# Kernel optimization log

Measured on AMD Instinct MI355X. Metric: run time of the kernel, lower is better.

The kernel has to match this reference:

```python
import jax, jax.numpy as jnp
import numpy as np


def setup_inputs() -> dict:
    key = jax.random.key(0)
    k1, k2, k3, k4 = jax.random.split(key, 4)
    num_tokens, hidden = 16384, 7168
    head_dim, coff = 512, 1            # compress_ratio=128 -> coff=1
    compress_ratio = 128
    num_blocks, block_size = 4096, 8   # block_size=8 for compress_ratio=128
    x = jax.random.normal(k1, (num_tokens, hidden), jnp.float32) * 0.02
    W = jax.random.normal(k2, (2 * coff * head_dim, hidden), jnp.float32) * 0.02
    ape = jax.random.normal(k3, (compress_ratio, coff * head_dim), jnp.float32)
    state_cache = jnp.zeros((num_blocks, block_size, 2 * coff * head_dim), jnp.float32)
    positions = jax.random.randint(k4, (num_tokens,), 0, 131072, dtype=jnp.int32)
    slot_mapping = jnp.arange(num_tokens, dtype=jnp.int32)  # unique, in-range slots
    return {"x": x, "W": W, "ape": ape, "state_cache": state_cache,
            "positions": positions, "slot_mapping": slot_mapping, "block_size": 8}


def reference(x, W, ape, state_cache, positions, slot_mapping, block_size):
    # fused_wkv_wgate GEMM (cublas bf16->fp32 in original): [T,H] @ [H,2D] -> [T,2D]
    kv_score = jnp.einsum('th,dh->td', x, W)
    D = W.shape[0] // 2                      # coff * head_dim (state_width)
    kv, score = kv_score[:, :D], kv_score[:, D:]
    compress_ratio = ape.shape[0]
    # fused APE lookup: ape[position % COMPRESS_RATIO] added to score half
    ape_rows = ape[positions % compress_ratio]          # [T, D]
    new_vals = jnp.concatenate([kv, score + ape_rows], axis=-1)  # [T, 2D]
    num_blocks, bs, width = state_cache.shape
    # slot -> (block_idx, pos_in_block) is exactly flat indexing for a
    # contiguous [num_blocks, block_size, width] cache.
    flat = state_cache.reshape(num_blocks * bs, width)
    # slot < 0 tokens are skipped (mapped out of range + mode='drop')
    idx = jnp.where(slot_mapping >= 0, slot_mapping, num_blocks * bs)
    flat = flat.at[idx].set(new_vals, mode='drop')
    return flat.reshape(num_blocks, bs, width)
```

## Files before the change

kernel.cpp:

```cpp
#include <hip/hip_runtime.h>
#include <hip/hip_bf16.h>
#include <stdint.h>


typedef short  bf16x8 __attribute__((ext_vector_type(8)));
typedef float  f32x4  __attribute__((ext_vector_type(4)));

#define BM 128
#define BN 128
#define BK 32
#define NT 256

#define GBM 256
#define GBN 256
#define GBK 64
#define GNT 512

__device__ __forceinline__ uint32_t pack_bf16x2(float lo, float hi) {
    uint32_t a = __float_as_uint(lo);
    uint32_t b = __float_as_uint(hi);
    a += 0x7fffu + ((a >> 16) & 1u);
    b += 0x7fffu + ((b >> 16) & 1u);
    return (a >> 16) | (b & 0xffff0000u);
}

__device__ __forceinline__ void gload_lds16(const uint16_t* g, uint16_t* l) {
    __builtin_amdgcn_global_load_lds(
        (const __attribute__((address_space(1))) uint32_t*)g,
        (__attribute__((address_space(3))) uint32_t*)l,
        16, 0, 0);
}

__global__ void set_flags(const int* __restrict__ slots, uint8_t* __restrict__ flags,
                          int num_tokens, int num_slots) {
    const int i = blockIdx.x * blockDim.x + threadIdx.x;
    if (i < num_tokens) {
        const int s = slots[i];
        if (s >= 0 && s < num_slots) flags[s] = 1;
    }
}

__global__ void prep(const float4* __restrict__ cache, float4* __restrict__ out,
                     const uint8_t* __restrict__ flags,
                     const float4* __restrict__ x, uint4* __restrict__ xb,
                     const float4* __restrict__ w, uint4* __restrict__ wb,
                     int n_c4, int nx8, int nw8) {
    const int i = blockIdx.x * blockDim.x + threadIdx.x;
    if (i < n_c4) {
        if (!flags[i >> 8]) out[i] = cache[i];
    } else if (i < n_c4 + nx8) {
        const int j = i - n_c4;
        const float4 a = x[2 * j];
        const float4 b = x[2 * j + 1];
        uint4 o;
        o.x = pack_bf16x2(a.x, a.y);
        o.y = pack_bf16x2(a.z, a.w);
        o.z = pack_bf16x2(b.x, b.y);
        o.w = pack_bf16x2(b.z, b.w);
        xb[j] = o;
    } else if (i < n_c4 + nx8 + nw8) {
        const int j = i - n_c4 - nx8;
        const float4 a = w[2 * j];
        const float4 b = w[2 * j + 1];
        uint4 o;
        o.x = pack_bf16x2(a.x, a.y);
        o.y = pack_bf16x2(a.z, a.w);
        o.z = pack_bf16x2(b.x, b.y);
        o.w = pack_bf16x2(b.z, b.w);
        wb[j] = o;
    }
}

__global__ __launch_bounds__(GNT, 2)
void gemm_bf16_scatter_256(const uint16_t* __restrict__ XB, const uint16_t* __restrict__ WB,
                           const float* __restrict__ ape, const int* __restrict__ positions,
                           const int* __restrict__ slots, float* __restrict__ out,
                           int K, int D, int CR, int num_slots, int n_tiles_m, int n_tiles_n)
{
    __shared__ uint16_t lds[2 * 2 * GBM * GBK];

    const int t    = threadIdx.x;
    const int lane = t & 63;
    const int wid  = t >> 6;
    const int wr   = wid >> 2;
    const int wc   = wid & 3;
    const int fr   = lane & 15;
    const int fc4  = lane >> 4;

    const int nblk = n_tiles_m * n_tiles_n;
    int tidx = blockIdx.x;
    if ((nblk & 7) == 0) {
        const int per = nblk >> 3;
        tidx = (tidx & 7) * per + (tidx >> 3);
    }
    const int tile_m = tidx / n_tiles_n;
    const int tile_n = tidx % n_tiles_n;

    const int rr = t >> 3;
    const int cs = ((t & 7) ^ (rr & 7)) * 8;
    const uint16_t* gA = XB + (size_t)(tile_m * GBM + rr) * K + cs;
    const uint16_t* gB = WB + (size_t)(tile_n * GBN + rr) * K + cs;
    uint16_t* const dst0 = lds + t * 8;

    const int c0 = (fc4 ^ (fr & 7)) * 8;
    const int c1 = ((4 + fc4) ^ (fr & 7)) * 8;
    const int arow0 = (wr * 128 + fr) * GBK;
    const int brow0 = (wc * 64 + fr) * GBK;

    f32x4 acc[8][4];
    #pragma unroll
    for (int i = 0; i < 8; i++)
        #pragma unroll
        for (int j = 0; j < 4; j++)
            acc[i][j] = f32x4{0.f, 0.f, 0.f, 0.f};

    const int nkt = K / GBK;

#define STAGE256(cur_, kt_) do {                                            \
    uint16_t* dA_ = dst0 + (cur_) * (2 * GBM * GBK);                        \
    uint16_t* dB_ = dA_ + (GBM * GBK);                                      \
    const size_t ko_ = (size_t)(kt_) * GBK;                                 \
    _Pragma("unroll")                                                       \
    for (int q_ = 0; q_ < 4; q_++) {                                        \
        gload_lds16(gA + ko_ + (size_t)q_ * 64 * K, dA_ + q_ * 4096);       \
        gload_lds16(gB + ko_ + (size_t)q_ * 64 * K, dB_ + q_ * 4096);       \
    }                                                                       \
} while (0)

    STAGE256(0, 0);
    if (nkt > 1) STAGE256(1, 1);

    for (int kt = 0; kt < nkt; ++kt) {
        const int cur = kt & 1;
        if (kt + 1 < nkt) asm volatile("s_waitcnt vmcnt(8)" ::: "memory");
        else              asm volatile("s_waitcnt vmcnt(0)" ::: "memory");
        __builtin_amdgcn_s_barrier();
        asm volatile("" ::: "memory");
        __builtin_amdgcn_sched_barrier(0);

        const uint16_t* A = lds + cur * (2 * GBM * GBK);
        const uint16_t* B = A + GBM * GBK;

        #pragma unroll
        for (int h = 0; h < 2; ++h) {
            const int cN = h ? c1 : c0;
            bf16x8 bfr[4];
            #pragma unroll
            for (int j = 0; j < 4; ++j)
                bfr[j] = *(const bf16x8*)(B + brow0 + j * (16 * GBK) + cN);
            #pragma unroll
            for (int mh = 0; mh < 2; ++mh) {
                bf16x8 afr[4];
                #pragma unroll
                for (int i = 0; i < 4; ++i)
                    afr[i] = *(const bf16x8*)(A + arow0 + mh * (64 * GBK) + i * (16 * GBK) + cN);
                __builtin_amdgcn_s_setprio(1);
                #pragma unroll
                for (int i = 0; i < 4; ++i)
                    #pragma unroll
                    for (int j = 0; j < 4; ++j)
                        acc[mh * 4 + i][j] = __builtin_amdgcn_mfma_f32_16x16x32_bf16(
                            afr[i], bfr[j], acc[mh * 4 + i][j], 0, 0, 0);
                __builtin_amdgcn_s_setprio(0);
            }
        }

        __builtin_amdgcn_sched_barrier(0);
        asm volatile("" ::: "memory");
        __builtin_amdgcn_s_barrier();
        asm volatile("" ::: "memory");
        __builtin_amdgcn_sched_barrier(0);
        if (kt + 2 < nkt) STAGE256(cur, kt + 2);
    }
#undef STAGE256

    const int D2 = 2 * D;
    const int mbase = tile_m * GBM + wr * 128 + fc4 * 4;
    const int nbase = tile_n * GBN + wc * 64 + fr;
    #pragma unroll
    for (int ai = 0; ai < 8; ++ai) {
        #pragma unroll
        for (int r = 0; r < 4; ++r) {
            const int token = mbase + ai * 16 + r;
            const int slot  = slots[token];
            if (slot < 0 || slot >= num_slots) continue;
            int p = positions[token];
            p = (CR & (CR - 1)) ? (p % CR) : (p & (CR - 1));
            const float* aperow = ape + (size_t)p * D;
            float* orow = out + (size_t)slot * D2;
            #pragma unroll
            for (int j = 0; j < 4; ++j) {
                const int col = nbase + j * 16;
                float v = acc[ai][j][r];
                if (col >= D) v += aperow[col - D];
                orow[col] = v;
            }
        }
    }
}

__global__ __launch_bounds__(NT, 4)
void gemm_bf16_scatter(const uint16_t* __restrict__ XB, const uint16_t* __restrict__ WB,
                       const float* __restrict__ ape, const int* __restrict__ positions,
                       const int* __restrict__ slots, float* __restrict__ out,
                       int K, int D, int CR, int num_slots, int n_tiles_m)
{
    __shared__ uint16_t ldsA[BM * BK];
    __shared__ uint16_t ldsB[BN * BK];

    const int tile_m = blockIdx.x % n_tiles_m;
    const int tile_n = blockIdx.x / n_tiles_m;
    const int t    = threadIdx.x;
    const int lane = t & 63;
    const int wid  = t >> 6;
    const int wm   = (wid >> 1) * 64;
    const int wn   = (wid & 1) * 64;
    const int fr   = lane & 15;
    const int fc   = lane >> 4;
    const int swz  = (fc ^ ((fr >> 1) & 3)) << 3;

    const int p0 = t, p1 = t + NT;
    const int r0 = p0 >> 2, c0 = (p0 & 3) ^ ((r0 >> 1) & 3);
    const int r1 = p1 >> 2, c1 = (p1 & 3) ^ ((r1 >> 1) & 3);

    const uint16_t* gA0 = XB + (size_t)(tile_m * BM + r0) * K + c0 * 8;
    const uint16_t* gA1 = XB + (size_t)(tile_m * BM + r1) * K + c1 * 8;
    const uint16_t* gB0 = WB + (size_t)(tile_n * BN + r0) * K + c0 * 8;
    const uint16_t* gB1 = WB + (size_t)(tile_n * BN + r1) * K + c1 * 8;
    uint16_t* lA0 = &ldsA[p0 * 8];
    uint16_t* lA1 = &ldsA[p1 * 8];
    uint16_t* lB0 = &ldsB[p0 * 8];
    uint16_t* lB1 = &ldsB[p1 * 8];

    f32x4 acc[4][4];
    #pragma unroll
    for (int i = 0; i < 4; i++)
        #pragma unroll
        for (int j = 0; j < 4; j++)
            acc[i][j] = f32x4{0.f, 0.f, 0.f, 0.f};

    for (int k0 = 0; k0 < K; k0 += BK) {
        gload_lds16(gA0 + k0, lA0);
        gload_lds16(gA1 + k0, lA1);
        gload_lds16(gB0 + k0, lB0);
        gload_lds16(gB1 + k0, lB1);
        __syncthreads();

        bf16x8 af[4], bfrag[4];
        #pragma unroll
        for (int i = 0; i < 4; i++)
            af[i] = *(const bf16x8*)&ldsA[(wm + i * 16 + fr) * BK + swz];
        #pragma unroll
        for (int j = 0; j < 4; j++)
            bfrag[j] = *(const bf16x8*)&ldsB[(wn + j * 16 + fr) * BK + swz];

        #pragma unroll
        for (int i = 0; i < 4; i++)
            #pragma unroll
            for (int j = 0; j < 4; j++)
                acc[i][j] = __builtin_amdgcn_mfma_f32_16x16x32_bf16(af[i], bfrag[j], acc[i][j], 0, 0, 0);
        __syncthreads();
    }

    const int D2 = 2 * D;
    #pragma unroll
    for (int i = 0; i < 4; i++) {
        #pragma unroll
        for (int r = 0; r < 4; r++) {
            const int token = tile_m * BM + wm + i * 16 + fc * 4 + r;
            const int slot  = slots[token];
            if (slot < 0 || slot >= num_slots) continue;
            const int p = positions[token] % CR;
            const float* aperow = ape + (size_t)p * D;
            float* orow = out + (size_t)slot * D2;
            #pragma unroll
            for (int j = 0; j < 4; j++) {
                const int col = tile_n * BN + wn + j * 16 + fr;
                float v = acc[i][j][r];
                if (col >= D) v += aperow[col - D];
                orow[col] = v;
            }
        }
    }
}

__global__ void copy_cache(const float4* __restrict__ src, float4* __restrict__ dst, int n4) {
    const int i = blockIdx.x * blockDim.x + threadIdx.x;
    if (i < n4) dst[i] = src[i];
}

__device__ __forceinline__ int lds_idx_f(int row, int chunk) {
    return row * BK + ((chunk ^ ((row >> 1) & 3)) << 3);
}

__global__ __launch_bounds__(NT, 2)
void gemm_scatter_f32(const float* __restrict__ X, const float* __restrict__ Wm,
                      const float* __restrict__ ape, const int* __restrict__ positions,
                      const int* __restrict__ slots, float* __restrict__ out,
                      int K, int D, int CR, int num_slots, int n_tiles_n)
{
    __shared__ uint16_t ldsA[BM * BK];
    __shared__ uint16_t ldsB[BN * BK];

    const int tile_m = blockIdx.x / n_tiles_n;
    const int tile_n = blockIdx.x % n_tiles_n;
    const int t    = threadIdx.x;
    const int lane = t & 63;
    const int wid  = t >> 6;
    const int wm   = (wid >> 1) * 64;
    const int wn   = (wid & 1) * 64;
    const int fr   = lane & 15;
    const int fc   = lane >> 4;
    const int swz  = fc ^ ((fr >> 1) & 3);

    const float* Abase = X  + (size_t)(tile_m * BM) * K;
    const float* Bbase = Wm + (size_t)(tile_n * BN) * K;

    f32x4 acc[4][4];
    #pragma unroll
    for (int i = 0; i < 4; i++)
        #pragma unroll
        for (int j = 0; j < 4; j++)
            acc[i][j] = f32x4{0.f, 0.f, 0.f, 0.f};

    for (int k0 = 0; k0 < K; k0 += BK) {
        #pragma unroll
        for (int i = 0; i < 4; i++) {
            const int lin = t + i * NT;
            const int row = lin >> 3;
            const int c4  = lin & 7;
            const int half = c4 & 1;
            const int sidx = lds_idx_f(row, c4 >> 1) + half * 4;

            const float4 va = *(const float4*)(Abase + (size_t)row * K + k0 + c4 * 4);
            uint2 pa; pa.x = pack_bf16x2(va.x, va.y); pa.y = pack_bf16x2(va.z, va.w);
            *(uint2*)&ldsA[sidx] = pa;

            const float4 vb = *(const float4*)(Bbase + (size_t)row * K + k0 + c4 * 4);
            uint2 pb; pb.x = pack_bf16x2(vb.x, vb.y); pb.y = pack_bf16x2(vb.z, vb.w);
            *(uint2*)&ldsB[sidx] = pb;
        }
        __syncthreads();

        bf16x8 af[4], bfrag[4];
        #pragma unroll
        for (int i = 0; i < 4; i++)
            af[i] = *(const bf16x8*)&ldsA[(wm + i * 16 + fr) * BK + (swz << 3)];
        #pragma unroll
        for (int j = 0; j < 4; j++)
            bfrag[j] = *(const bf16x8*)&ldsB[(wn + j * 16 + fr) * BK + (swz << 3)];

        #pragma unroll
        for (int i = 0; i < 4; i++)
            #pragma unroll
            for (int j = 0; j < 4; j++)
                acc[i][j] = __builtin_amdgcn_mfma_f32_16x16x32_bf16(af[i], bfrag[j], acc[i][j], 0, 0, 0);
        __syncthreads();
    }

    const int D2 = 2 * D;
    #pragma unroll
    for (int i = 0; i < 4; i++) {
        #pragma unroll
        for (int r = 0; r < 4; r++) {
            const int token = tile_m * BM + wm + i * 16 + fc * 4 + r;
            const int slot  = slots[token];
            if (slot < 0 || slot >= num_slots) continue;
            const int p = positions[token] % CR;
            const float* aperow = ape + (size_t)p * D;
            float* orow = out + (size_t)slot * D2;
            #pragma unroll
            for (int j = 0; j < 4; j++) {
                const int col = tile_n * BN + wn + j * 16 + fr;
                float v = acc[i][j][r];
                if (col >= D) v += aperow[col - D];
                orow[col] = v;
            }
        }
    }
}

extern "C" void kernel_launch(void* const* d_in, const int* in_sizes, int n_in,
                              void* d_out, int out_size, void* d_ws, size_t ws_size,
                              hipStream_t stream) {
    const float* x         = (const float*)d_in[0];
    const float* W         = (const float*)d_in[1];
    const float* ape       = (const float*)d_in[2];
    const float* cache     = (const float*)d_in[3];
    const int*   positions = (const int*)d_in[4];
    const int*   slots     = (const int*)d_in[5];
    float* out = (float*)d_out;

    const int num_tokens = in_sizes[4];
    const int hidden     = in_sizes[0] / num_tokens;
    const int D2         = in_sizes[1] / hidden;
    const int D          = D2 / 2;
    const int CR         = in_sizes[2] / D;
    const int num_slots  = in_sizes[3] / D2;

    const int n_tiles_m = num_tokens / BM;
    const int n_tiles_n = D2 / BN;

    const size_t nx = (size_t)in_sizes[0];
    const size_t nw = (size_t)in_sizes[1];
    const size_t need = (nx + nw) * sizeof(uint16_t) + (size_t)num_slots;

    if (ws_size >= need) {
        uint16_t* xb = (uint16_t*)d_ws;
        uint16_t* wb = xb + nx;
        uint8_t* flags = (uint8_t*)(wb + nw);

        hipMemsetAsync(flags, 0, num_slots, stream);
        set_flags<<<(num_tokens + 255) / 256, 256, 0, stream>>>(slots, flags, num_tokens, num_slots);

        const int n_c4 = out_size / 4;
        const int nx8  = (int)(nx / 8);
        const int nw8  = (int)(nw / 8);
        const int total = n_c4 + nx8 + nw8;
        prep<<<(total + 255) / 256, 256, 0, stream>>>(
            (const float4*)cache, (float4*)out, flags,
            (const float4*)x, (uint4*)xb, (const float4*)W, (uint4*)wb,
            n_c4, nx8, nw8);

        const bool div256 = (num_tokens % GBM == 0) && (D2 % GBN == 0) &&
                            (hidden % GBK == 0) && (hidden / GBK >= 1);
        if (div256) {
            const int tm = num_tokens / GBM;
            const int tn = D2 / GBN;
            gemm_bf16_scatter_256<<<tm * tn, GNT, 0, stream>>>(
                xb, wb, ape, positions, slots, out, hidden, D, CR, num_slots, tm, tn);
        } else {
            gemm_bf16_scatter<<<n_tiles_m * n_tiles_n, NT, 0, stream>>>(
                xb, wb, ape, positions, slots, out, hidden, D, CR, num_slots, n_tiles_m);
        }
    } else {
        const int n4 = out_size / 4;
        copy_cache<<<(n4 + 255) / 256, 256, 0, stream>>>((const float4*)cache, (float4*)out, n4);
        gemm_scatter_f32<<<n_tiles_m * n_tiles_n, NT, 0, stream>>>(
            x, W, ape, positions, slots, out, hidden, D, CR, num_slots, n_tiles_n);
    }
}
```

Measured before the change: 997.4 us.

## Fuse fp32-to-bf16 conversion and cache copy into the 256-tile GEMM

The new GEMM kernel loads fp32 X and W straight from global memory into registers, converts them to bf16 and writes them to LDS with register double-buffering. This replaces the separate prep pass that wrote bf16 copies to the workspace. The unflagged cache-row copy also moves into the GEMM kernel's tail as a grid-stride loop. This removes a kernel launch and the bf16 round-trip through memory. In exchange the GEMM reads twice the bytes per tile, loses async direct-to-LDS loads, and holds more registers for staging.

```diff
diff --git a/kernel.cpp b/kernel.cpp
--- a/kernel.cpp
+++ b/kernel.cpp
@@ -37,6 +37,179 @@
     if (i < num_tokens) {
         const int s = slots[i];
         if (s >= 0 && s < num_slots) flags[s] = 1;
+    }
+}
+
+__global__ __launch_bounds__(GNT, 2)
+void gemm_fused_256(const float* __restrict__ X, const float* __restrict__ Wm,
+                    const float* __restrict__ ape, const int* __restrict__ positions,
+                    const int* __restrict__ slots, const float4* __restrict__ cache4,
+                    const uint8_t* __restrict__ flags, float* __restrict__ out,
+                    int K, int D, int CR, int num_slots, int n_tiles_m, int n_tiles_n)
+{
+    __shared__ uint16_t lds[2 * 2 * GBM * GBK];
+
+    const int t    = threadIdx.x;
+    const int lane = t & 63;
+    const int wid  = t >> 6;
+    const int wr   = wid >> 2;
+    const int wc   = wid & 3;
+    const int fr   = lane & 15;
+    const int fc4  = lane >> 4;
+
+    const int nblk = n_tiles_m * n_tiles_n;
+    int tidx = blockIdx.x;
+    if ((nblk & 7) == 0) {
+        const int per = nblk >> 3;
+        tidx = (tidx & 7) * per + (tidx >> 3);
+    }
+    const int tile_m = tidx / n_tiles_n;
+    const int tile_n = tidx % n_tiles_n;
+
+    const int srow = t >> 3;
+    const int c    = t & 7;
+    const int swzc = c ^ (srow & 7);
+    const float* gA = X  + (size_t)(tile_m * GBM + srow) * K + c * 8;
+    const float* gB = Wm + (size_t)(tile_n * GBN + srow) * K + c * 8;
+    uint16_t* const wA0 = lds + srow * GBK + swzc * 8;
+
+    const int c0 = (fc4 ^ (fr & 7)) * 8;
+    const int c1 = ((4 + fc4) ^ (fr & 7)) * 8;
+    const int arow0 = (wr * 128 + fr) * GBK;
+    const int brow0 = (wc * 64 + fr) * GBK;
+
+    float4 ra[4][2], rb[4][2];
+
+    f32x4 acc[8][4];
+    #pragma unroll
+    for (int i = 0; i < 8; i++)
+        #pragma unroll
+        for (int j = 0; j < 4; j++)
+            acc[i][j] = f32x4{0.f, 0.f, 0.f, 0.f};
+
+    const int nkt = K / GBK;
+
+#define LOADT(kt_) do {                                                       \
+    const size_t ko_ = (size_t)(kt_) * GBK;                                   \
+    _Pragma("unroll")                                                         \
+    for (int q_ = 0; q_ < 4; q_++) {                                          \
+        ra[q_][0] = *(const float4*)(gA + ko_ + (size_t)q_ * 64 * K);         \
+        ra[q_][1] = *(const float4*)(gA + ko_ + (size_t)q_ * 64 * K + 4);     \
+        rb[q_][0] = *(const float4*)(gB + ko_ + (size_t)q_ * 64 * K);         \
+        rb[q_][1] = *(const float4*)(gB + ko_ + (size_t)q_ * 64 * K + 4);     \
+    }                                                                         \
+} while (0)
+
+#define WRITET(buf_) do {                                                     \
+    uint16_t* bA_ = wA0 + (buf_) * (2 * GBM * GBK);                           \
+    uint16_t* bB_ = bA_ + GBM * GBK;                                          \
+    _Pragma("unroll")                                                         \
+    for (int q_ = 0; q_ < 4; q_++) {                                          \
+        uint4 oa_, ob_;                                                       \
+        oa_.x = pack_bf16x2(ra[q_][0].x, ra[q_][0].y);                        \
+        oa_.y = pack_bf16x2(ra[q_][0].z, ra[q_][0].w);                        \
+        oa_.z = pack_bf16x2(ra[q_][1].x, ra[q_][1].y);                        \
+        oa_.w = pack_bf16x2(ra[q_][1].z, ra[q_][1].w);                        \
+        *(uint4*)(bA_ + q_ * 64 * GBK) = oa_;                                 \
+        ob_.x = pack_bf16x2(rb[q_][0].x, rb[q_][0].y);                        \
+        ob_.y = pack_bf16x2(rb[q_][0].z, rb[q_][0].w);                        \
+        ob_.z = pack_bf16x2(rb[q_][1].x, rb[q_][1].y);                        \
+        ob_.w = pack_bf16x2(rb[q_][1].z, rb[q_][1].w);                        \
+        *(uint4*)(bB_ + q_ * 64 * GBK) = ob_;                                 \
+    }                                                                         \
+} while (0)
+
+    LOADT(0);
+    WRITET(0);
+    if (nkt > 1) LOADT(1);
+    asm volatile("s_waitcnt lgkmcnt(0)" ::: "memory");
+    __builtin_amdgcn_sched_barrier(0);
+    __builtin_amdgcn_s_barrier();
+    asm volatile("" ::: "memory");
+    __builtin_amdgcn_sched_barrier(0);
+
+    for (int kt = 0; kt < nkt; ++kt) {
+        const int cur = kt & 1;
+        const uint16_t* A = lds + cur * (2 * GBM * GBK);
+        const uint16_t* B = A + GBM * GBK;
+
+        #pragma unroll
+        for (int h = 0; h < 2; ++h) {
+            const int cN = h ? c1 : c0;
+            bf16x8 bfr[4];
+            #pragma unroll
+            for (int j = 0; j < 4; ++j)
+                bfr[j] = *(const bf16x8*)(B + brow0 + j * (16 * GBK) + cN);
+            #pragma unroll
+            for (int mh = 0; mh < 2; ++mh) {
+                bf16x8 afr[4];
+                #pragma unroll
+                for (int i = 0; i < 4; ++i)
+                    afr[i] = *(const bf16x8*)(A + arow0 + mh * (64 * GBK) + i * (16 * GBK) + cN);
+                __builtin_amdgcn_s_setprio(1);
+                #pragma unroll
+                for (int i = 0; i < 4; ++i)
+                    #pragma unroll
+                    for (int j = 0; j < 4; ++j)
+                        acc[mh * 4 + i][j] = __builtin_amdgcn_mfma_f32_16x16x32_bf16(
+                            afr[i], bfr[j], acc[mh * 4 + i][j], 0, 0, 0);
+                __builtin_amdgcn_s_setprio(0);
+            }
+        }
+
+        if (kt + 1 < nkt) {
+            __builtin_amdgcn_sched_barrier(0);
+            WRITET(cur ^ 1);
+            if (kt + 2 < nkt) LOADT(kt + 2);
+            asm volatile("s_waitcnt lgkmcnt(0)" ::: "memory");
+            __builtin_amdgcn_sched_barrier(0);
+            __builtin_amdgcn_s_barrier();
+            asm volatile("" ::: "memory");
+            __builtin_amdgcn_sched_barrier(0);
+        }
+    }
+#undef LOADT
+#undef WRITET
+
+    const int D2 = 2 * D;
+    const int mbase = tile_m * GBM + wr * 128 + fc4 * 4;
+    const int nbase = tile_n * GBN + wc * 64 + fr;
+    #pragma unroll
+    for (int ai = 0; ai < 8; ++ai) {
+        #pragma unroll
+        for (int r = 0; r < 4; ++r) {
+            const int token = mbase + ai * 16 + r;
+            const int slot  = slots[token];
+            if (slot < 0 || slot >= num_slots) continue;
+            int p = positions[token];
+            p = (CR & (CR - 1)) ? (p % CR) : (p & (CR - 1));
+            const float* aperow = ape + (size_t)p * D;
+            float* orow = out + (size_t)slot * D2;
+            #pragma unroll
+            for (int j = 0; j < 4; ++j) {
+                const int col = nbase + j * 16;
+                float v = acc[ai][j][r];
+                if (col >= D) v += aperow[col - D];
+                orow[col] = v;
+            }
+        }
+    }
+
+    float4* out4 = (float4*)out;
+    const int rowlen4 = D2 >> 2;
+    if ((rowlen4 & (rowlen4 - 1)) == 0) {
+        int sh = 0;
+        while ((1 << sh) < rowlen4) ++sh;
+        const long total4 = (long)num_slots << sh;
+        for (long i = (long)blockIdx.x * GNT + t; i < total4; i += (long)gridDim.x * GNT)
+            if (!flags[i >> sh]) out4[i] = cache4[i];
+    } else {
+        for (int s = blockIdx.x; s < num_slots; s += gridDim.x) {
+            if (flags[s]) continue;
+            const float4* src = cache4 + (size_t)s * rowlen4;
+            float4* dst = out4 + (size_t)s * rowlen4;
+            for (int j = t; j < rowlen4; j += GNT) dst[j] = src[j];
+        }
     }
 }
 
@@ -71,134 +244,6 @@
     }
 }
 
-__global__ __launch_bounds__(GNT, 2)
-void gemm_bf16_scatter_256(const uint16_t* __restrict__ XB, const uint16_t* __restrict__ WB,
-                           const float* __restrict__ ape, const int* __restrict__ positions,
-                           const int* __restrict__ slots, float* __restrict__ out,
-                           int K, int D, int CR, int num_slots, int n_tiles_m, int n_tiles_n)
-{
-    __shared__ uint16_t lds[2 * 2 * GBM * GBK];
-
-    const int t    = threadIdx.x;
-    const int lane = t & 63;
-    const int wid  = t >> 6;
-    const int wr   = wid >> 2;
-    const int wc   = wid & 3;
-    const int fr   = lane & 15;
-    const int fc4  = lane >> 4;
-
-    const int nblk = n_tiles_m * n_tiles_n;
-    int tidx = blockIdx.x;
-    if ((nblk & 7) == 0) {
-        const int per = nblk >> 3;
-        tidx = (tidx & 7) * per + (tidx >> 3);
-    }
-    const int tile_m = tidx / n_tiles_n;
-    const int tile_n = tidx % n_tiles_n;
-
-    const int rr = t >> 3;
-    const int cs = ((t & 7) ^ (rr & 7)) * 8;
-    const uint16_t* gA = XB + (size_t)(tile_m * GBM + rr) * K + cs;
-    const uint16_t* gB = WB + (size_t)(tile_n * GBN + rr) * K + cs;
-    uint16_t* const dst0 = lds + t * 8;
-
-    const int c0 = (fc4 ^ (fr & 7)) * 8;
-    const int c1 = ((4 + fc4) ^ (fr & 7)) * 8;
-    const int arow0 = (wr * 128 + fr) * GBK;
-    const int brow0 = (wc * 64 + fr) * GBK;
-
-    f32x4 acc[8][4];
-    #pragma unroll
-    for (int i = 0; i < 8; i++)
-        #pragma unroll
-        for (int j = 0; j < 4; j++)
-            acc[i][j] = f32x4{0.f, 0.f, 0.f, 0.f};
-
-    const int nkt = K / GBK;
-
-#define STAGE256(cur_, kt_) do {                                            \
-    uint16_t* dA_ = dst0 + (cur_) * (2 * GBM * GBK);                        \
-    uint16_t* dB_ = dA_ + (GBM * GBK);                                      \
-    const size_t ko_ = (size_t)(kt_) * GBK;                                 \
-    _Pragma("unroll")                                                       \
-    for (int q_ = 0; q_ < 4; q_++) {                                        \
-        gload_lds16(gA + ko_ + (size_t)q_ * 64 * K, dA_ + q_ * 4096);       \
-        gload_lds16(gB + ko_ + (size_t)q_ * 64 * K, dB_ + q_ * 4096);       \
-    }                                                                       \
-} while (0)
-
-    STAGE256(0, 0);
-    if (nkt > 1) STAGE256(1, 1);
-
-    for (int kt = 0; kt < nkt; ++kt) {
-        const int cur = kt & 1;
-        if (kt + 1 < nkt) asm volatile("s_waitcnt vmcnt(8)" ::: "memory");
-        else              asm volatile("s_waitcnt vmcnt(0)" ::: "memory");
-        __builtin_amdgcn_s_barrier();
-        asm volatile("" ::: "memory");
-        __builtin_amdgcn_sched_barrier(0);
-
-        const uint16_t* A = lds + cur * (2 * GBM * GBK);
-        const uint16_t* B = A + GBM * GBK;
-
-        #pragma unroll
-        for (int h = 0; h < 2; ++h) {
-            const int cN = h ? c1 : c0;
-            bf16x8 bfr[4];
-            #pragma unroll
-            for (int j = 0; j < 4; ++j)
-                bfr[j] = *(const bf16x8*)(B + brow0 + j * (16 * GBK) + cN);
-            #pragma unroll
-            for (int mh = 0; mh < 2; ++mh) {
-                bf16x8 afr[4];
-                #pragma unroll
-                for (int i = 0; i < 4; ++i)
-                    afr[i] = *(const bf16x8*)(A + arow0 + mh * (64 * GBK) + i * (16 * GBK) + cN);
-                __builtin_amdgcn_s_setprio(1);
-                #pragma unroll
-                for (int i = 0; i < 4; ++i)
-                    #pragma unroll
-                    for (int j = 0; j < 4; ++j)
-                        acc[mh * 4 + i][j] = __builtin_amdgcn_mfma_f32_16x16x32_bf16(
-                            afr[i], bfr[j], acc[mh * 4 + i][j], 0, 0, 0);
-                __builtin_amdgcn_s_setprio(0);
-            }
-        }
-
-        __builtin_amdgcn_sched_barrier(0);
-        asm volatile("" ::: "memory");
-        __builtin_amdgcn_s_barrier();
-        asm volatile("" ::: "memory");
-        __builtin_amdgcn_sched_barrier(0);
-        if (kt + 2 < nkt) STAGE256(cur, kt + 2);
-    }
-#undef STAGE256
-
-    const int D2 = 2 * D;
-    const int mbase = tile_m * GBM + wr * 128 + fc4 * 4;
-    const int nbase = tile_n * GBN + wc * 64 + fr;
-    #pragma unroll
-    for (int ai = 0; ai < 8; ++ai) {
-        #pragma unroll
-        for (int r = 0; r < 4; ++r) {
-            const int token = mbase + ai * 16 + r;
-            const int slot  = slots[token];
-            if (slot < 0 || slot >= num_slots) continue;
-            int p = positions[token];
-            p = (CR & (CR - 1)) ? (p % CR) : (p & (CR - 1));
-            const float* aperow = ape + (size_t)p * D;
-            float* orow = out + (size_t)slot * D2;
-            #pragma unroll
-            for (int j = 0; j < 4; ++j) {
-                const int col = nbase + j * 16;
-                float v = acc[ai][j][r];
-                if (col >= D) v += aperow[col - D];
-                orow[col] = v;
-            }
-        }
-    }
-}
-
 __global__ __launch_bounds__(NT, 4)
 void gemm_bf16_scatter(const uint16_t* __restrict__ XB, const uint16_t* __restrict__ WB,
                        const float* __restrict__ ape, const int* __restrict__ positions,
@@ -220,13 +265,13 @@
     const int swz  = (fc ^ ((fr >> 1) & 3)) << 3;
 
     const int p0 = t, p1 = t + NT;
-    const int r0 = p0 >> 2, c0 = (p0 & 3) ^ ((r0 >> 1) & 3);
-    const int r1 = p1 >> 2, c1 = (p1 & 3) ^ ((r1 >> 1) & 3);
-
-    const uint16_t* gA0 = XB + (size_t)(tile_m * BM + r0) * K + c0 * 8;
-    const uint16_t* gA1 = XB + (size_t)(tile_m * BM + r1) * K + c1 * 8;
-    const uint16_t* gB0 = WB + (size_t)(tile_n * BN + r0) * K + c0 * 8;
-    const uint16_t* gB1 = WB + (size_t)(tile_n * BN + r1) * K + c1 * 8;
+    const int r0 = p0 >> 2, cc0 = (p0 & 3) ^ ((r0 >> 1) & 3);
+    const int r1 = p1 >> 2, cc1 = (p1 & 3) ^ ((r1 >> 1) & 3);
+
+    const uint16_t* gA0 = XB + (size_t)(tile_m * BM + r0) * K + cc0 * 8;
+    const uint16_t* gA1 = XB + (size_t)(tile_m * BM + r1) * K + cc1 * 8;
+    const uint16_t* gB0 = WB + (size_t)(tile_n * BN + r0) * K + cc0 * 8;
+    const uint16_t* gB1 = WB + (size_t)(tile_n * BN + r1) * K + cc1 * 8;
     uint16_t* lA0 = &ldsA[p0 * 8];
     uint16_t* lA1 = &ldsA[p1 * 8];
     uint16_t* lB0 = &ldsB[p0 * 8];
@@ -403,9 +448,21 @@
 
     const size_t nx = (size_t)in_sizes[0];
     const size_t nw = (size_t)in_sizes[1];
-    const size_t need = (nx + nw) * sizeof(uint16_t) + (size_t)num_slots;
-
-    if (ws_size >= need) {
+    const size_t need_old = (nx + nw) * sizeof(uint16_t) + (size_t)num_slots;
+
+    const bool div256 = (num_tokens % GBM == 0) && (D2 % GBN == 0) && (hidden % GBK == 0);
+
+    if (div256 && ws_size >= (size_t)num_slots) {
+        uint8_t* flags = (uint8_t*)d_ws;
+        hipMemsetAsync(flags, 0, num_slots, stream);
+        set_flags<<<(num_tokens + 255) / 256, 256, 0, stream>>>(slots, flags, num_tokens, num_slots);
+
+        const int tm = num_tokens / GBM;
+        const int tn = D2 / GBN;
+        gemm_fused_256<<<tm * tn, GNT, 0, stream>>>(
+            x, W, ape, positions, slots, (const float4*)cache, flags, out,
+            hidden, D, CR, num_slots, tm, tn);
+    } else if (ws_size >= need_old) {
         uint16_t* xb = (uint16_t*)d_ws;
         uint16_t* wb = xb + nx;
         uint8_t* flags = (uint8_t*)(wb + nw);
@@ -422,17 +479,8 @@
             (const float4*)x, (uint4*)xb, (const float4*)W, (uint4*)wb,
             n_c4, nx8, nw8);
 
-        const bool div256 = (num_tokens % GBM == 0) && (D2 % GBN == 0) &&
-                            (hidden % GBK == 0) && (hidden / GBK >= 1);
-        if (div256) {
-            const int tm = num_tokens / GBM;
-            const int tn = D2 / GBN;
-            gemm_bf16_scatter_256<<<tm * tn, GNT, 0, stream>>>(
-                xb, wb, ape, positions, slots, out, hidden, D, CR, num_slots, tm, tn);
-        } else {
-            gemm_bf16_scatter<<<n_tiles_m * n_tiles_n, NT, 0, stream>>>(
-                xb, wb, ape, positions, slots, out, hidden, D, CR, num_slots, n_tiles_m);
-        }
+        gemm_bf16_scatter<<<n_tiles_m * n_tiles_n, NT, 0, stream>>>(
+            xb, wb, ape, positions, slots, out, hidden, D, CR, num_slots, n_tiles_m);
     } else {
         const int n4 = out_size / 4;
         copy_cache<<<(n4 + 255) / 256, 256, 0, stream>>>((const float4*)cache, (float4*)out, n4);
```

Result: no change. 1.013 ms (+1.6%).
